# Kernel tuning notes

Measured on AMD Instinct MI355X. Metric: run time of the kernel, lower is better.

The kernel has to match this reference:

```python
import jax, jax.numpy as jnp
import numpy as np

N_NODES = 100000


def _gcn_norm(edge_index, num_nodes):
    # PyG GCNConv: add self-loops, symmetric normalization deg^-1/2 A deg^-1/2
    loops = jnp.arange(num_nodes, dtype=edge_index.dtype)
    src = jnp.concatenate([edge_index[0], loops])
    dst = jnp.concatenate([edge_index[1], loops])
    deg = jax.ops.segment_sum(jnp.ones_like(dst, dtype=jnp.float32), dst,
                              num_segments=num_nodes)
    dinv = jnp.where(deg > 0, jax.lax.rsqrt(deg), 0.0)
    norm = dinv[src] * dinv[dst]  # [E + N]
    return src, dst, norm


def _gcn_conv(x, src, dst, norm, W, b, num_nodes):
    h = x @ W                                   # [N, out]
    msg = h[src] * norm[:, None]                # gather + scale  [E+N, out]
    agg = jax.ops.segment_sum(msg, dst, num_segments=num_nodes)  # scatter-add
    return agg + b


def setup_inputs() -> dict:
    key = jax.random.key(0)
    k = jax.random.split(key, 8)
    nfeat, nhid, E = 256, 128, 1600000
    x = jax.random.normal(k[0], (N_NODES, nfeat), dtype=jnp.float32)
    edge_index = jax.random.randint(k[1], (2, E), 0, N_NODES, dtype=jnp.int32)
    # Glorot-style params (GCNConv weights + biases), Linear(nhid,1) xavier + zero bias
    s1 = float(np.sqrt(6.0 / (nfeat + nhid)))
    s2 = float(np.sqrt(6.0 / (nhid + nhid)))
    sf = float(np.sqrt(6.0 / (nhid + 1)))
    W1 = jax.random.uniform(k[2], (nfeat, nhid), jnp.float32, -s1, s1)
    b1 = jnp.zeros((nhid,), jnp.float32)
    W2 = jax.random.uniform(k[3], (nhid, nhid), jnp.float32, -s2, s2)
    b2 = jnp.zeros((nhid,), jnp.float32)
    Wf = jax.random.uniform(k[4], (nhid, 1), jnp.float32, -sf, sf)
    bf = jnp.zeros((1,), jnp.float32)
    return {"x": x, "edge_index": edge_index, "W1": W1, "b1": b1,
            "W2": W2, "b2": b2, "Wf": Wf, "bf": bf}


def reference(x, edge_index, W1, b1, W2, b2, Wf, bf):
    n = x.shape[0]
    src, dst, norm = _gcn_norm(edge_index, n)
    h = jax.nn.relu(_gcn_conv(x, src, dst, norm, W1, b1, n))
    # dropout is identity at inference
    h = _gcn_conv(h, src, dst, norm, W2, b2, n)
    out = h @ Wf + bf            # Linear(nhid, 1)
    return out.squeeze(-1)       # [N]
```

## Files before the change

### kernel.cpp

```cpp
#include <hip/hip_runtime.h>
#include <hip/hip_bf16.h>

#define NF 256
#define NH 128
#define PSZ_SH 7
#define MAXP 1024
#define NCB 512

typedef __attribute__((ext_vector_type(8))) short short8;
typedef __attribute__((ext_vector_type(4))) float float4v;

static __device__ __forceinline__ ushort f2bf(float f) {
  unsigned u = __float_as_uint(f);
  u = (u + 0x7fffu + ((u >> 16) & 1u)) >> 16;
  return (ushort)u;
}
static __device__ __forceinline__ float bflo(unsigned u) { return __uint_as_float(u << 16); }
static __device__ __forceinline__ float bfhi(unsigned u) { return __uint_as_float(u & 0xffff0000u); }

static __device__ __forceinline__ short8 pack_bf8(float4 v0, float4 v1) {
  short8 r;
  r[0] = (short)f2bf(v0.x); r[1] = (short)f2bf(v0.y);
  r[2] = (short)f2bf(v0.z); r[3] = (short)f2bf(v0.w);
  r[4] = (short)f2bf(v1.x); r[5] = (short)f2bf(v1.y);
  r[6] = (short)f2bf(v1.z); r[7] = (short)f2bf(v1.w);
  return r;
}

__global__ __launch_bounds__(256) void k_initall(
    const int* __restrict__ ei, int E, int P, int* __restrict__ bcnt, int chunk,
    const float* __restrict__ W1, ushort* __restrict__ Wfr,
    const float* __restrict__ W2, const float* __restrict__ Wfv,
    const float* __restrict__ b2, const float* __restrict__ bfv,
    float* __restrict__ Wc) {
  int b = blockIdx.x;
  if (b < 128) {
    int g = b * 256 + threadIdx.x;
    int ii   = g & 7;
    int lane = (g >> 3) & 63;
    int t    = (g >> 9) & 7;
    int ks   = g >> 12;
    int k = ks * 32 + ((lane >> 4) << 3) + ii;
    int c = t * 16 + (lane & 15);
    Wfr[g] = f2bf(W1[(size_t)k * NH + c]);
  } else if (b == 128) {
    __shared__ float wl[NH];
    if (threadIdx.x < NH) wl[threadIdx.x] = Wfv[threadIdx.x];
    __syncthreads();
    if (threadIdx.x < NH) {
      int i = threadIdx.x;
      const float4* w4 = reinterpret_cast<const float4*>(&W2[(size_t)i * NH]);
      float s = 0.f;
#pragma unroll 8
      for (int k = 0; k < NH / 4; ++k) {
        float4 v = w4[k];
        s += v.x * wl[4 * k] + v.y * wl[4 * k + 1] + v.z * wl[4 * k + 2] + v.w * wl[4 * k + 3];
      }
      Wc[i] = s;
      if (i == 0) {
        float c = 0.f;
        for (int k = 0; k < NH; ++k) c += b2[k] * wl[k];
        Wc[NH] = c + bfv[0];
      }
    }
  } else {
    int cb = b - 129;
    __shared__ int hc[MAXP];
    for (int j = threadIdx.x; j < P; j += 256) hc[j] = 0;
    __syncthreads();
    int start = cb * chunk;
    int endE = min(start + chunk, E);
    if ((E & 3) == 0 && (start & 3) == 0) {
      int nvec = (endE - start) >> 2;
      const int4* dst4 = reinterpret_cast<const int4*>(&ei[E + start]);
      for (int q = threadIdx.x; q < nvec; q += 256) {
        int4 d = dst4[q];
        atomicAdd(&hc[d.x >> PSZ_SH], 1);
        atomicAdd(&hc[d.y >> PSZ_SH], 1);
        atomicAdd(&hc[d.z >> PSZ_SH], 1);
        atomicAdd(&hc[d.w >> PSZ_SH], 1);
      }
      for (int e = start + (nvec << 2) + (int)threadIdx.x; e < endE; e += 256)
        atomicAdd(&hc[ei[E + e] >> PSZ_SH], 1);
    } else {
      for (int e = start + (int)threadIdx.x; e < endE; e += 256)
        atomicAdd(&hc[ei[E + e] >> PSZ_SH], 1);
    }
    __syncthreads();
    for (int j = threadIdx.x; j < P; j += 256) bcnt[cb * P + j] = hc[j];
  }
}

__global__ __launch_bounds__(NCB) void k_scanA(const int* __restrict__ bcnt,
                                               int* __restrict__ bloc,
                                               int* __restrict__ ptot, int P) {
  __shared__ int ws[NCB / 64];
  int p = blockIdx.x, tid = threadIdx.x, lane = tid & 63, wid = tid >> 6;
  int v = bcnt[tid * P + p];
  int pre = v;
#pragma unroll
  for (int m = 1; m < 64; m <<= 1) {
    int t = __shfl_up(pre, m, 64);
    if (lane >= m) pre += t;
  }
  if (lane == 63) ws[wid] = pre;
  __syncthreads();
  if (tid == 0) {
    int run = 0;
#pragma unroll
    for (int j = 0; j < NCB / 64; ++j) { int t = ws[j]; ws[j] = run; run += t; }
    ptot[p] = run;
  }
  __syncthreads();
  bloc[tid * P + p] = ws[wid] + pre - v;
}

__global__ __launch_bounds__(1024) void k_scanB(const int* __restrict__ ptot,
                                                int* __restrict__ pbase, int P, int E) {
  __shared__ int ws[16];
  int tid = threadIdx.x, lane = tid & 63, wid = tid >> 6;
  int v = (tid < P) ? ptot[tid] : 0;
  int pre = v;
#pragma unroll
  for (int m = 1; m < 64; m <<= 1) {
    int t = __shfl_up(pre, m, 64);
    if (lane >= m) pre += t;
  }
  if (lane == 63) ws[wid] = pre;
  __syncthreads();
  if (tid == 0) {
    int run = 0;
#pragma unroll
    for (int j = 0; j < 16; ++j) { int t = ws[j]; ws[j] = run; run += t; }
  }
  __syncthreads();
  if (tid < P) pbase[tid] = ws[wid] + pre - v;
  if (tid == 0) pbase[P] = E;
}

__global__ __launch_bounds__(256) void k_scatter(const int* __restrict__ ei, int E,
                                                 const int* __restrict__ pbase,
                                                 const int* __restrict__ bloc,
                                                 uint* __restrict__ sub, int chunk, int P) {
  __shared__ int cur[MAXP];
  int b = blockIdx.x;
  for (int j = threadIdx.x; j < P; j += 256) cur[j] = pbase[j] + bloc[b * P + j];
  __syncthreads();
  int start = b * chunk;
  int endE = min(start + chunk, E);
  if ((E & 3) == 0 && (start & 3) == 0) {
    int nvec = (endE - start) >> 2;
    const int4* src4 = reinterpret_cast<const int4*>(&ei[start]);
    const int4* dst4 = reinterpret_cast<const int4*>(&ei[E + start]);
    for (int q = threadIdx.x; q < nvec; q += 256) {
      int4 s = src4[q];
      int4 d = dst4[q];
      int p0 = atomicAdd(&cur[d.x >> PSZ_SH], 1);
      sub[p0] = (uint)s.x | ((uint)(d.x & ((1 << PSZ_SH) - 1)) << 20);
      int p1 = atomicAdd(&cur[d.y >> PSZ_SH], 1);
      sub[p1] = (uint)s.y | ((uint)(d.y & ((1 << PSZ_SH) - 1)) << 20);
      int p2 = atomicAdd(&cur[d.z >> PSZ_SH], 1);
      sub[p2] = (uint)s.z | ((uint)(d.z & ((1 << PSZ_SH) - 1)) << 20);
      int p3 = atomicAdd(&cur[d.w >> PSZ_SH], 1);
      sub[p3] = (uint)s.w | ((uint)(d.w & ((1 << PSZ_SH) - 1)) << 20);
    }
    for (int e = start + (nvec << 2) + (int)threadIdx.x; e < endE; e += 256) {
      int s = ei[e];
      int d = ei[E + e];
      int pos = atomicAdd(&cur[d >> PSZ_SH], 1);
      sub[pos] = (uint)s | ((uint)(d & ((1 << PSZ_SH) - 1)) << 20);
    }
  } else {
    for (int e = start + (int)threadIdx.x; e < endE; e += 256) {
      int s = ei[e];
      int d = ei[E + e];
      int pos = atomicAdd(&cur[d >> PSZ_SH], 1);
      sub[pos] = (uint)s | ((uint)(d & ((1 << PSZ_SH) - 1)) << 20);
    }
  }
}

__global__ __launch_bounds__(256) void k_bucket(const uint* __restrict__ sub,
                                                const int* __restrict__ pbase,
                                                int* __restrict__ rowptr, int* __restrict__ deg,
                                                float* __restrict__ dinv, int* __restrict__ csr,
                                                int N) {
  __shared__ int hist[1 << PSZ_SH];
  __shared__ int curL[1 << PSZ_SH];
  __shared__ int wsum[2];
  const int p = blockIdx.x, tid = threadIdx.x;
  const int base = pbase[p];
  const int cnt = pbase[p + 1] - base;
  const int node0 = p << PSZ_SH;
  if (tid < (1 << PSZ_SH)) hist[tid] = 0;
  __syncthreads();
  for (int e = tid; e < cnt; e += 256) atomicAdd(&hist[sub[base + e] >> 20], 1);
  __syncthreads();
  int d = 0, pre = 0;
  if (tid < (1 << PSZ_SH)) {
    d = hist[tid];
    pre = d;
#pragma unroll
    for (int m = 1; m < 64; m <<= 1) {
      int t = __shfl_up(pre, m, 64);
      if ((tid & 63) >= m) pre += t;
    }
    if ((tid & 63) == 63) wsum[tid >> 6] = pre;
  }
  __syncthreads();
  if (tid < (1 << PSZ_SH)) {
    int excl = base + ((tid >= 64) ? wsum[0] : 0) + pre - d;
    curL[tid] = excl;
    int node = node0 + tid;
    if (node < N) {
      rowptr[node] = excl;
      deg[node] = d;
      dinv[node] = rsqrtf((float)d + 1.0f);
    }
  }
  __syncthreads();
  for (int e = tid; e < cnt; e += 256) {
    uint v = sub[base + e];
    int pos = atomicAdd(&curL[v >> 20], 1);
    csr[pos] = (int)(v & 0xFFFFFu);
  }
}

__global__ __launch_bounds__(256, 2) void k_gemm1(
    const float* __restrict__ x, const ushort* __restrict__ Wf,
    const float* __restrict__ dinv, ushort* __restrict__ hs, int N) {
  __shared__ ushort Ol[64][136];
  const int tid = threadIdx.x;
  const int w = tid >> 6, l = tid & 63;
  const int row0 = blockIdx.x * 64;
  const int arow = row0 + 16 * w + (l & 15);
  const int kg = l >> 4;
  const bool rv = arow < N;
  const float* xr = &x[(size_t)(rv ? arow : 0) * NF + kg * 8];

  float4 xf0[8], xf1[8];
#pragma unroll
  for (int ks = 0; ks < 8; ++ks) {
    xf0[ks] = *reinterpret_cast<const float4*>(&xr[ks * 32]);
    xf1[ks] = *reinterpret_cast<const float4*>(&xr[ks * 32 + 4]);
  }
  __builtin_amdgcn_sched_barrier(0);

  short8 afr[8];
#pragma unroll
  for (int ks = 0; ks < 8; ++ks) {
    float4 v0 = xf0[ks], v1 = xf1[ks];
    if (!rv) { v0 = make_float4(0.f, 0.f, 0.f, 0.f); v1 = v0; }
    afr[ks] = pack_bf8(v0, v1);
  }

  const short8* Wb = reinterpret_cast<const short8*>(Wf);
  float4v acc[8];
#pragma unroll
  for (int t = 0; t < 8; ++t) acc[t] = (float4v){0.f, 0.f, 0.f, 0.f};
  short8 bc[8], bn[8];
#pragma unroll
  for (int ks = 0; ks < 8; ++ks) bc[ks] = Wb[(ks * 8 + 0) * 64 + l];
#pragma unroll
  for (int tp = 0; tp < 4; ++tp) {
    const int t0 = 2 * tp, t1 = 2 * tp + 1;
#pragma unroll
    for (int ks = 0; ks < 8; ++ks) bn[ks] = Wb[(ks * 8 + t1) * 64 + l];
    __builtin_amdgcn_sched_barrier(0);
#pragma unroll
    for (int ks = 0; ks < 8; ++ks)
      acc[t0] = __builtin_amdgcn_mfma_f32_16x16x32_bf16(afr[ks], bc[ks], acc[t0], 0, 0, 0);
    if (tp < 3) {
#pragma unroll
      for (int ks = 0; ks < 8; ++ks) bc[ks] = Wb[(ks * 8 + t1 + 1) * 64 + l];
      __builtin_amdgcn_sched_barrier(0);
    }
#pragma unroll
    for (int ks = 0; ks < 8; ++ks)
      acc[t1] = __builtin_amdgcn_mfma_f32_16x16x32_bf16(afr[ks], bn[ks], acc[t1], 0, 0, 0);
  }

  float dj[4];
#pragma unroll
  for (int j = 0; j < 4; ++j) {
    int grow = row0 + 16 * w + (l >> 4) * 4 + j;
    dj[j] = (grow < N) ? dinv[grow] : 0.f;
  }
#pragma unroll
  for (int t = 0; t < 8; ++t)
#pragma unroll
    for (int j = 0; j < 4; ++j)
      Ol[16 * w + (l >> 4) * 4 + j][16 * t + (l & 15)] = f2bf(acc[t][j] * dj[j]);
  __syncthreads();
  {
    const int r = tid >> 2, grow = row0 + r;
    if (grow < N) {
      uint* dsts = (uint*)hs;
#pragma unroll
      for (int q = 0; q < 4; ++q) {
        uint4 v = *reinterpret_cast<const uint4*>(&Ol[r][(tid & 3) * 32 + q * 8]);
        *reinterpret_cast<uint4*>(&dsts[(size_t)grow * 64 + (tid & 3) * 16 + q * 4]) = v;
      }
    }
  }
}

static __device__ __forceinline__ void accg(float2* a, uint4 u) {
  a[0].x += __uint_as_float(u.x << 16); a[0].y += __uint_as_float(u.x);
  a[1].x += __uint_as_float(u.y << 16); a[1].y += __uint_as_float(u.y);
  a[2].x += __uint_as_float(u.z << 16); a[2].y += __uint_as_float(u.z);
  a[3].x += __uint_as_float(u.w << 16); a[3].y += __uint_as_float(u.w);
}

__global__ __launch_bounds__(256) void k_agg1_z(
    const uint4* __restrict__ hs4, const int* __restrict__ rowptr,
    const int* __restrict__ deg, const int* __restrict__ csr,
    const float* __restrict__ dinv, const float* __restrict__ b1,
    const float* __restrict__ Wc, float* __restrict__ zs,
    float* __restrict__ out, int N) {
  int g = blockIdx.x * blockDim.x + threadIdx.x;
  int i = g >> 6;
  if (i >= N) return;
  int lane = threadIdx.x & 63;
  int q = lane >> 4;
  int sub = lane & 15;

  float2 a2[4];
  {
    uint4 u = hs4[(size_t)i * 16 + sub];
    if (q) { u.x = 0u; u.y = 0u; u.z = 0u; u.w = 0u; }
    a2[0] = make_float2(bflo(u.x), bfhi(u.x));
    a2[1] = make_float2(bflo(u.y), bfhi(u.y));
    a2[2] = make_float2(bflo(u.z), bfhi(u.z));
    a2[3] = make_float2(bflo(u.w), bfhi(u.w));
  }

  int kk = rowptr[i];
  const int end = kk + deg[i];
  for (; kk + 15 < end; kk += 16) {
    int c0 = csr[kk + q];
    int c1 = csr[kk + 4 + q];
    int c2 = csr[kk + 8 + q];
    int c3 = csr[kk + 12 + q];
    uint4 u0 = hs4[(size_t)c0 * 16 + sub];
    uint4 u1 = hs4[(size_t)c1 * 16 + sub];
    uint4 u2 = hs4[(size_t)c2 * 16 + sub];
    uint4 u3 = hs4[(size_t)c3 * 16 + sub];
    accg(a2, u0); accg(a2, u1); accg(a2, u2); accg(a2, u3);
  }
  for (; kk + 3 < end; kk += 4) {
    int c = csr[kk + q];
    uint4 u = hs4[(size_t)c * 16 + sub];
    accg(a2, u);
  }
  int r = end - kk;
  if (r > 0) {
    int c = csr[kk + (q < r ? q : r - 1)];
    uint4 u = hs4[(size_t)c * 16 + sub];
    if (q >= r) { u.x = 0u; u.y = 0u; u.z = 0u; u.w = 0u; }
    accg(a2, u);
  }

  float a[8] = {a2[0].x, a2[0].y, a2[1].x, a2[1].y, a2[2].x, a2[2].y, a2[3].x, a2[3].y};
#pragma unroll
  for (int j = 0; j < 8; ++j) {
    a[j] += __shfl_xor(a[j], 16, 64);
    a[j] += __shfl_xor(a[j], 32, 64);
  }

  float d = dinv[i];
  float4 ba = reinterpret_cast<const float4*>(b1)[2 * sub];
  float4 bb = reinterpret_cast<const float4*>(b1)[2 * sub + 1];
  float4 wa = reinterpret_cast<const float4*>(Wc)[2 * sub];
  float4 wb = reinterpret_cast<const float4*>(Wc)[2 * sub + 1];
  float s = fmaxf(fmaf(d, a[0], ba.x), 0.f) * wa.x
          + fmaxf(fmaf(d, a[1], ba.y), 0.f) * wa.y
          + fmaxf(fmaf(d, a[2], ba.z), 0.f) * wa.z
          + fmaxf(fmaf(d, a[3], ba.w), 0.f) * wa.w
          + fmaxf(fmaf(d, a[4], bb.x), 0.f) * wb.x
          + fmaxf(fmaf(d, a[5], bb.y), 0.f) * wb.y
          + fmaxf(fmaf(d, a[6], bb.z), 0.f) * wb.z
          + fmaxf(fmaf(d, a[7], bb.w), 0.f) * wb.w;
#pragma unroll
  for (int m = 8; m >= 1; m >>= 1) s += __shfl_xor(s, m, 64);
  if (lane == 0) {
    float zsv = d * s;
    zs[i] = zsv;
    out[i] = d * zsv + Wc[NH];
  }
}

__global__ void k_out2(const int* __restrict__ rowptr, const int* __restrict__ deg,
                       const int* __restrict__ csr, const float* __restrict__ zs,
                       const float* __restrict__ dinv, float* __restrict__ out, int N) {
  int i = blockIdx.x * blockDim.x + threadIdx.x;
  if (i >= N) return;
  int k = rowptr[i], end = k + deg[i];
  float s = 0.f;
  for (; k + 3 < end; k += 4) {
    float t0 = zs[csr[k]], t1 = zs[csr[k + 1]], t2 = zs[csr[k + 2]], t3 = zs[csr[k + 3]];
    s += (t0 + t1) + (t2 + t3);
  }
  for (; k < end; ++k) s += zs[csr[k]];
  out[i] += dinv[i] * s;
}

extern "C" void kernel_launch(void* const* d_in, const int* in_sizes, int n_in,
                              void* d_out, int out_size, void* d_ws, size_t ws_size,
                              hipStream_t stream) {
  const float* x  = (const float*)d_in[0];
  const int*   ei = (const int*)d_in[1];
  const float* W1 = (const float*)d_in[2];
  const float* b1 = (const float*)d_in[3];
  const float* W2 = (const float*)d_in[4];
  const float* b2 = (const float*)d_in[5];
  const float* Wf = (const float*)d_in[6];
  const float* bf = (const float*)d_in[7];
  const int N = in_sizes[0] / NF;
  const int E = in_sizes[1] / 2;
  const int P = (N + (1 << PSZ_SH) - 1) >> PSZ_SH;
  const int chunk = (((E + NCB - 1) / NCB) + 3) & ~3;

  char* ws = (char*)d_ws;
  size_t off = 0;
  auto alloc = [&](size_t bytes) {
    void* p = ws + off;
    off = (off + bytes + 255) & ~(size_t)255;
    return p;
  };
  ushort* hs     = (ushort*)alloc((size_t)N * NH * 2);
  ushort* Wfrag  = (ushort*)alloc((size_t)NF * NH * 2);
  int*    csr    = (int*)alloc((size_t)E * 4);
  uint*   sub    = (uint*)alloc((size_t)E * 4);
  int*    deg    = (int*)alloc((size_t)N * 4);
  int*    rowptr = (int*)alloc((size_t)N * 4);
  float*  dinv   = (float*)alloc((size_t)N * 4);
  float*  zs     = (float*)alloc((size_t)N * 4);
  float*  Wc     = (float*)alloc(132 * 4);
  int*    bcnt   = (int*)alloc((size_t)NCB * P * 4);
  int*    bloc   = (int*)alloc((size_t)NCB * P * 4);
  int*    ptot   = (int*)alloc((size_t)P * 4);
  int*    pbase  = (int*)alloc((size_t)(P + 1) * 4);
  float*  out    = (float*)d_out;

  const int b = 256;
  k_initall<<<129 + NCB, b, 0, stream>>>(ei, E, P, bcnt, chunk,
                                         W1, Wfrag, W2, Wf, b2, bf, Wc);
  k_scanA  <<<P, NCB, 0, stream>>>(bcnt, bloc, ptot, P);
  k_scanB  <<<1, 1024, 0, stream>>>(ptot, pbase, P, E);
  k_scatter<<<NCB, b, 0, stream>>>(ei, E, pbase, bloc, sub, chunk, P);
  k_bucket <<<P, b, 0, stream>>>(sub, pbase, rowptr, deg, dinv, csr, N);
  k_gemm1  <<<(N + 63) / 64, 256, 0, stream>>>(x, Wfrag, dinv, hs, N);
  k_agg1_z <<<(int)(((size_t)N * 64 + b - 1) / b), b, 0, stream>>>(
      (const uint4*)hs, rowptr, deg, csr, dinv, b1, Wc, zs, out, N);
  k_out2   <<<(N + b - 1) / b, b, 0, stream>>>(rowptr, deg, csr, zs, dinv, out, N);
}
```

Measured before the change: 157.4 us.

## Split GEMM K-loop into halves, widen bucket blocks, unroll out2 gather

The GEMM kernel now loads and converts the x row in two K halves, overlapping the second half's global loads with the first half's MFMAs. This cuts live registers so occupancy can rise to 3 blocks per SIMD. The bucket kernel runs with 512 threads per block instead of 256, and the final gather kernel unrolls by 8 with two accumulators for more memory-level parallelism. Risks include register spills under the tighter launch bound and more atomic contention on the shared histogram with the larger blocks.

```diff
diff --git a/kernel.cpp b/kernel.cpp
--- a/kernel.cpp
+++ b/kernel.cpp
@@ -180,7 +180,7 @@
   }
 }
 
-__global__ __launch_bounds__(256) void k_bucket(const uint* __restrict__ sub,
+__global__ __launch_bounds__(512) void k_bucket(const uint* __restrict__ sub,
                                                 const int* __restrict__ pbase,
                                                 int* __restrict__ rowptr, int* __restrict__ deg,
                                                 float* __restrict__ dinv, int* __restrict__ csr,
@@ -194,7 +194,7 @@
   const int node0 = p << PSZ_SH;
   if (tid < (1 << PSZ_SH)) hist[tid] = 0;
   __syncthreads();
-  for (int e = tid; e < cnt; e += 256) atomicAdd(&hist[sub[base + e] >> 20], 1);
+  for (int e = tid; e < cnt; e += 512) atomicAdd(&hist[sub[base + e] >> 20], 1);
   __syncthreads();
   int d = 0, pre = 0;
   if (tid < (1 << PSZ_SH)) {
@@ -219,14 +219,14 @@
     }
   }
   __syncthreads();
-  for (int e = tid; e < cnt; e += 256) {
+  for (int e = tid; e < cnt; e += 512) {
     uint v = sub[base + e];
     int pos = atomicAdd(&curL[v >> 20], 1);
     csr[pos] = (int)(v & 0xFFFFFu);
   }
 }
 
-__global__ __launch_bounds__(256, 2) void k_gemm1(
+__global__ __launch_bounds__(256, 3) void k_gemm1(
     const float* __restrict__ x, const ushort* __restrict__ Wf,
     const float* __restrict__ dinv, ushort* __restrict__ hs, int N) {
   __shared__ ushort Ol[64][136];
@@ -237,47 +237,76 @@
   const int kg = l >> 4;
   const bool rv = arow < N;
   const float* xr = &x[(size_t)(rv ? arow : 0) * NF + kg * 8];
-
-  float4 xf0[8], xf1[8];
-#pragma unroll
-  for (int ks = 0; ks < 8; ++ks) {
-    xf0[ks] = *reinterpret_cast<const float4*>(&xr[ks * 32]);
-    xf1[ks] = *reinterpret_cast<const float4*>(&xr[ks * 32 + 4]);
+  const short8* Wb = reinterpret_cast<const short8*>(Wf);
+
+  float4v acc[8];
+#pragma unroll
+  for (int t = 0; t < 8; ++t) acc[t] = (float4v){0.f, 0.f, 0.f, 0.f};
+
+  float4 xf[8];
+#pragma unroll
+  for (int ks = 0; ks < 4; ++ks) {
+    xf[2 * ks]     = *reinterpret_cast<const float4*>(&xr[ks * 32]);
+    xf[2 * ks + 1] = *reinterpret_cast<const float4*>(&xr[ks * 32 + 4]);
   }
   __builtin_amdgcn_sched_barrier(0);
-
-  short8 afr[8];
-#pragma unroll
-  for (int ks = 0; ks < 8; ++ks) {
-    float4 v0 = xf0[ks], v1 = xf1[ks];
+  short8 afr0[4];
+#pragma unroll
+  for (int ks = 0; ks < 4; ++ks) {
+    float4 v0 = xf[2 * ks], v1 = xf[2 * ks + 1];
     if (!rv) { v0 = make_float4(0.f, 0.f, 0.f, 0.f); v1 = v0; }
-    afr[ks] = pack_bf8(v0, v1);
-  }
-
-  const short8* Wb = reinterpret_cast<const short8*>(Wf);
-  float4v acc[8];
-#pragma unroll
-  for (int t = 0; t < 8; ++t) acc[t] = (float4v){0.f, 0.f, 0.f, 0.f};
-  short8 bc[8], bn[8];
-#pragma unroll
-  for (int ks = 0; ks < 8; ++ks) bc[ks] = Wb[(ks * 8 + 0) * 64 + l];
-#pragma unroll
-  for (int tp = 0; tp < 4; ++tp) {
-    const int t0 = 2 * tp, t1 = 2 * tp + 1;
-#pragma unroll
-    for (int ks = 0; ks < 8; ++ks) bn[ks] = Wb[(ks * 8 + t1) * 64 + l];
-    __builtin_amdgcn_sched_barrier(0);
-#pragma unroll
-    for (int ks = 0; ks < 8; ++ks)
-      acc[t0] = __builtin_amdgcn_mfma_f32_16x16x32_bf16(afr[ks], bc[ks], acc[t0], 0, 0, 0);
-    if (tp < 3) {
-#pragma unroll
-      for (int ks = 0; ks < 8; ++ks) bc[ks] = Wb[(ks * 8 + t1 + 1) * 64 + l];
+    afr0[ks] = pack_bf8(v0, v1);
+  }
+#pragma unroll
+  for (int ks = 0; ks < 4; ++ks) {
+    xf[2 * ks]     = *reinterpret_cast<const float4*>(&xr[(ks + 4) * 32]);
+    xf[2 * ks + 1] = *reinterpret_cast<const float4*>(&xr[(ks + 4) * 32 + 4]);
+  }
+  __builtin_amdgcn_sched_barrier(0);
+
+  {
+    short8 bc[4], bn[4];
+#pragma unroll
+    for (int ks = 0; ks < 4; ++ks) bc[ks] = Wb[(ks * 8 + 0) * 64 + l];
+#pragma unroll
+    for (int t = 0; t < 8; ++t) {
+      if (t < 7) {
+#pragma unroll
+        for (int ks = 0; ks < 4; ++ks) bn[ks] = Wb[(ks * 8 + t + 1) * 64 + l];
+      }
       __builtin_amdgcn_sched_barrier(0);
-    }
-#pragma unroll
-    for (int ks = 0; ks < 8; ++ks)
-      acc[t1] = __builtin_amdgcn_mfma_f32_16x16x32_bf16(afr[ks], bn[ks], acc[t1], 0, 0, 0);
+#pragma unroll
+      for (int ks = 0; ks < 4; ++ks)
+        acc[t] = __builtin_amdgcn_mfma_f32_16x16x32_bf16(afr0[ks], bc[ks], acc[t], 0, 0, 0);
+#pragma unroll
+      for (int ks = 0; ks < 4; ++ks) bc[ks] = bn[ks];
+    }
+  }
+
+  short8 afr1[4];
+#pragma unroll
+  for (int ks = 0; ks < 4; ++ks) {
+    float4 v0 = xf[2 * ks], v1 = xf[2 * ks + 1];
+    if (!rv) { v0 = make_float4(0.f, 0.f, 0.f, 0.f); v1 = v0; }
+    afr1[ks] = pack_bf8(v0, v1);
+  }
+  {
+    short8 bc[4], bn[4];
+#pragma unroll
+    for (int ks = 0; ks < 4; ++ks) bc[ks] = Wb[((ks + 4) * 8 + 0) * 64 + l];
+#pragma unroll
+    for (int t = 0; t < 8; ++t) {
+      if (t < 7) {
+#pragma unroll
+        for (int ks = 0; ks < 4; ++ks) bn[ks] = Wb[((ks + 4) * 8 + t + 1) * 64 + l];
+      }
+      __builtin_amdgcn_sched_barrier(0);
+#pragma unroll
+      for (int ks = 0; ks < 4; ++ks)
+        acc[t] = __builtin_amdgcn_mfma_f32_16x16x32_bf16(afr1[ks], bc[ks], acc[t], 0, 0, 0);
+#pragma unroll
+      for (int ks = 0; ks < 4; ++ks) bc[ks] = bn[ks];
+    }
   }
 
   float dj[4];
@@ -396,13 +425,17 @@
   int i = blockIdx.x * blockDim.x + threadIdx.x;
   if (i >= N) return;
   int k = rowptr[i], end = k + deg[i];
-  float s = 0.f;
-  for (; k + 3 < end; k += 4) {
-    float t0 = zs[csr[k]], t1 = zs[csr[k + 1]], t2 = zs[csr[k + 2]], t3 = zs[csr[k + 3]];
-    s += (t0 + t1) + (t2 + t3);
-  }
-  for (; k < end; ++k) s += zs[csr[k]];
-  out[i] += dinv[i] * s;
+  float s0 = 0.f, s1 = 0.f;
+  for (; k + 7 < end; k += 8) {
+    float t0 = zs[csr[k]],     t1 = zs[csr[k + 1]];
+    float t2 = zs[csr[k + 2]], t3 = zs[csr[k + 3]];
+    float t4 = zs[csr[k + 4]], t5 = zs[csr[k + 5]];
+    float t6 = zs[csr[k + 6]], t7 = zs[csr[k + 7]];
+    s0 += (t0 + t1) + (t2 + t3);
+    s1 += (t4 + t5) + (t6 + t7);
+  }
+  for (; k < end; ++k) s0 += zs[csr[k]];
+  out[i] += dinv[i] * (s0 + s1);
 }
 
 extern "C" void kernel_launch(void* const* d_in, const int* in_sizes, int n_in,
@@ -449,7 +482,7 @@
   k_scanA  <<<P, NCB, 0, stream>>>(bcnt, bloc, ptot, P);
   k_scanB  <<<1, 1024, 0, stream>>>(ptot, pbase, P, E);
   k_scatter<<<NCB, b, 0, stream>>>(ei, E, pbase, bloc, sub, chunk, P);
-  k_bucket <<<P, b, 0, stream>>>(sub, pbase, rowptr, deg, dinv, csr, N);
+  k_bucket <<<P, 512, 0, stream>>>(sub, pbase, rowptr, deg, dinv, csr, N);
   k_gemm1  <<<(N + 63) / 64, 256, 0, stream>>>(x, Wfrag, dinv, hs, N);
   k_agg1_z <<<(int)(((size_t)N * 64 + b - 1) / b), b, 0, stream>>>(
       (const uint4*)hs, rowptr, deg, csr, dinv, b1, Wc, zs, out, N);
```

Result: no change. 156.2 us (median of 2 runs) (-0.8%).
